# Kernel optimization log

Hardware: AMD Instinct MI355X
Metric: run time of the kernel (lower is better)

Reference implementation:

```python
import jax, jax.numpy as jnp
import numpy as np
import math

EMBED_DIM = 1024
NUM_HEADS = 16
HEAD_DIM = EMBED_DIM // NUM_HEADS
BLOCK_SIZE = 64
NUM_RAND_BLOCKS = 3
B, L = 2, 2048


def _build_sparse_mask(seq_len, block_size, num_rand_blocks, seed=0):
    """BigBird block-sparse mask: global (first/last block) + window (prev/self/next) + random blocks."""
    nb = seq_len // block_size
    bm = np.zeros((nb, nb), dtype=bool)
    # global: first and last blocks attend to all / are attended by all
    bm[0, :] = True
    bm[:, 0] = True
    bm[-1, :] = True
    bm[:, -1] = True
    # sliding window for interior blocks
    for b in range(1, nb - 1):
        bm[b, max(b - 1, 0):b + 2] = True
    # random blocks for interior blocks (deterministic for reproducibility)
    rng = np.random.default_rng(seed)
    for b in range(1, nb - 1):
        avail = [x for x in range(nb) if x != b]
        picks = rng.permutation(len(avail))[:num_rand_blocks]
        for p in picks:
            bm[b, avail[p]] = True
    # expand block mask to token-level [L, L]
    return np.kron(bm, np.ones((block_size, block_size), dtype=bool))


def setup_inputs() -> dict:
    key = jax.random.key(0)
    k0, k1, k2, k3, k4 = jax.random.split(key, 5)
    hidden_states = jax.random.normal(k0, (B, L, EMBED_DIM), dtype=jnp.float32)
    s = 0.02
    # torch nn.Linear weights have shape [out_features, in_features]
    Wq = jax.random.normal(k1, (EMBED_DIM, EMBED_DIM), dtype=jnp.float32) * s
    Wk = jax.random.normal(k2, (EMBED_DIM, EMBED_DIM), dtype=jnp.float32) * s
    Wv = jax.random.normal(k3, (EMBED_DIM, EMBED_DIM), dtype=jnp.float32) * s
    Wo = jax.random.normal(k4, (EMBED_DIM, EMBED_DIM), dtype=jnp.float32) * s
    sparse_mask = jnp.asarray(_build_sparse_mask(L, BLOCK_SIZE, NUM_RAND_BLOCKS))
    return {"hidden_states": hidden_states, "Wq": Wq, "Wk": Wk, "Wv": Wv,
            "Wo": Wo, "sparse_mask": sparse_mask}


def reference(hidden_states, Wq, Wk, Wv, Wo, sparse_mask):
    Bsz, Lq, D = hidden_states.shape
    H, hd = NUM_HEADS, HEAD_DIM
    # projections (Linear no bias): x @ W.T
    q = (hidden_states @ Wq.T).reshape(Bsz, Lq, H, hd).transpose(0, 2, 1, 3)
    k = (hidden_states @ Wk.T).reshape(Bsz, Lq, H, hd).transpose(0, 2, 1, 3)
    v = (hidden_states @ Wv.T).reshape(Bsz, Lq, H, hd).transpose(0, 2, 1, 3)
    # dense scores with block-sparse mask (matches reference module's math)
    scores = jnp.einsum('bhqd,bhkd->bhqk', q, k) / math.sqrt(hd)  # [B,H,L,L]
    scores = jnp.where(sparse_mask[None, None, :, :], scores, -jnp.inf)
    attn = jax.nn.softmax(scores.astype(jnp.float32), axis=-1).astype(scores.dtype)
    out = jnp.einsum('bhqk,bhkd->bhqd', attn, v)
    out = out.transpose(0, 2, 1, 3).reshape(Bsz, Lq, D)
    out = out @ Wo.T
    return out
```

## Files before the change

kernel.cpp:

```cpp
#include <hip/hip_runtime.h>
#include <hip/hip_bf16.h>
#include <stdint.h>

#define LSEQ   2048
#define DMODEL 1024
#define NHEADS 16
#define HDIM   64
#define NB     32
#define BATCH  2
#define NGRP   38
#define NWG_ATTN (32 * NGRP)

typedef unsigned short u16;
typedef __attribute__((ext_vector_type(8))) __bf16 bf16x8;
typedef __attribute__((ext_vector_type(4))) float f32x4;
typedef __attribute__((ext_vector_type(4))) unsigned int u32x4;
typedef __attribute__((ext_vector_type(4))) u16 u16x4;


__device__ __forceinline__ u16 f2b(float f) {
  unsigned b = __float_as_uint(f);
  return (u16)((b + 0x7FFFu + ((b >> 16) & 1u)) >> 16);
}

__device__ __forceinline__ void lds_dma16(const u16* g, u16* l) {
  __builtin_amdgcn_global_load_lds(
      (__attribute__((address_space(1))) const void*)g,
      (__attribute__((address_space(3))) void*)l, 16, 0, 0);
}

__device__ __forceinline__ bool probe_is_bf16(const void* src) {
  const u16* p = (const u16*)src;
  int cnt = 0;
  #pragma unroll
  for (int i = 0; i < 64; ++i) {
    int e = (p[i] >> 7) & 0xFF;
    cnt += (e >= 100 && e <= 140) ? 1 : 0;
  }
  return cnt >= 48;
}

__device__ __forceinline__ bool mask_block(const void* m, int qb, int kb) {
  const unsigned char* p = (const unsigned char*)m;
  size_t e = (size_t)(qb * 64) * LSEQ + (size_t)kb * 64;
  unsigned char b0 = p[0], b1 = p[1], b2 = p[2];
  if (b0 == 1 && b1 == 1) return p[e] != 0;
  if (b0 == 1 && b1 == 0 && b2 == 1) return ((const u16*)m)[e] != 0;
  if (b0 == 1) return ((const unsigned int*)m)[e] != 0;
  if (b0 == 0x80 && b1 == 0x3f) return ((const u16*)m)[e] != 0;
  return ((const float*)m)[e] != 0.0f;
}

__global__ __launch_bounds__(256) void convert_kernel(
    const void* __restrict__ hs, const void* __restrict__ wq,
    const void* __restrict__ wk, const void* __restrict__ wv,
    const void* __restrict__ wo, u16* __restrict__ dst,
    const void* __restrict__ mask, int* __restrict__ skb,
    f32x4* __restrict__ zbuf, int zn4) {
  if (blockIdx.x == 0 && threadIdx.x < NB) {
    int qb = threadIdx.x;
    int base = (qb == 0) ? 0 : ((qb == 31) ? 32 : (64 + (qb - 1) * 8));
    int cap = (qb == 0 || qb == 31) ? 32 : 8;
    int c = 0;
    for (int kb = 0; kb < NB; ++kb)
      if (mask_block(mask, qb, kb)) skb[base + c++] = kb;
    for (; c < cap; ++c) skb[base + c] = -1;
  }
  int stride = gridDim.x * blockDim.x;
  for (int i = blockIdx.x * blockDim.x + threadIdx.x; i < zn4; i += stride)
    zbuf[i] = (f32x4){0.f, 0.f, 0.f, 0.f};

  if (probe_is_bf16(hs)) return;

  const int HS4 = BATCH * LSEQ * DMODEL / 4;
  const int W4 = DMODEL * DMODEL / 4;
  int total4 = HS4 + 4 * W4;
  for (int i = blockIdx.x * blockDim.x + threadIdx.x; i < total4; i += stride) {
    const void* src;
    int off;
    if (i < HS4) { src = hs; off = i; }
    else {
      int j = i - HS4;
      int wsel = j >> 18;
      off = j & (W4 - 1);
      src = (wsel == 0) ? wq : (wsel == 1) ? wk : (wsel == 2) ? wv : wo;
    }
    f32x4 f = ((const f32x4*)src)[off];
    ((u16x4*)dst)[i] = (u16x4){f2b(f[0]), f2b(f[1]), f2b(f[2]), f2b(f[3])};
  }
}

#define GBK 32
#define TN  128

template <int TM>
__global__ __launch_bounds__(256) void gemm_bt(
    const void* __restrict__ probe_src,
    const u16* __restrict__ A_bf, const u16* __restrict__ A_alt,
    const u16* __restrict__ Braw0, const u16* __restrict__ Braw1,
    const u16* __restrict__ Braw2, const u16* __restrict__ Bconv,
    void* __restrict__ C, u16* __restrict__ C2, int N, int K, int layout) {
  constexpr int NJ = (TM == 128) ? 4 : 2;
  __shared__ u16 lA[TM * 32];
  __shared__ u16 lB[TN * 32];
  int t = threadIdx.x;
  int w = t >> 6, l = t & 63, q4 = l >> 4, lc = l & 15;
  int lr = l >> 2, lcc = l & 3;
  int tileM = blockIdx.x * TM, tileN = blockIdx.y * TN;
  int wm = (TM == 128) ? (w >> 1) * 64 : 0;
  int wn = (TM == 128) ? (w & 1) * 64 : w * 32;

  bool bf = probe_is_bf16(probe_src);
  const u16* A = bf ? A_bf : A_alt;
  const u16* Bbase;
  int bOff;
  if (bf) {
    Bbase = (tileN < 1024) ? Braw0 : (tileN < 2048) ? Braw1 : Braw2;
    bOff = tileN & 1023;
  } else {
    Bbase = Bconv;
    bOff = tileN;
  }

  f32x4 acc[4][NJ] = {};

  for (int kt = 0; kt < K; kt += GBK) {
    __syncthreads();
    #pragma unroll
    for (int it = 0; it < TM / 64; ++it) {
      int m = w * (TM / 64) + it;
      lds_dma16(A + (size_t)(tileM + m * 16 + lr) * K + kt + lcc * 8, lA + m * 512);
    }
    #pragma unroll
    for (int it = 0; it < 2; ++it) {
      int m = w * 2 + it;
      lds_dma16(Bbase + (size_t)(bOff + m * 16 + lr) * K + kt + lcc * 8, lB + m * 512);
    }
    __syncthreads();

    bf16x8 af[4], bfr[NJ];
    #pragma unroll
    for (int i = 0; i < 4; ++i)
      af[i] = *(const bf16x8*)(lA + (wm + i * 16 + lc) * 32 + q4 * 8);
    #pragma unroll
    for (int j = 0; j < NJ; ++j)
      bfr[j] = *(const bf16x8*)(lB + (wn + j * 16 + lc) * 32 + q4 * 8);
    #pragma unroll
    for (int i = 0; i < 4; ++i)
      #pragma unroll
      for (int j = 0; j < NJ; ++j)
        acc[i][j] = __builtin_amdgcn_mfma_f32_16x16x32_bf16(af[i], bfr[j], acc[i][j], 0, 0, 0);
  }

  bool out_bf = (layout == 1) ? true : bf;
  #pragma unroll
  for (int i = 0; i < 4; ++i)
    #pragma unroll
    for (int j = 0; j < NJ; ++j) {
      int rowb = tileM + wm + i * 16 + q4 * 4;
      int col = tileN + wn + j * 16 + lc;
      if (layout == 0) {
        #pragma unroll
        for (int r = 0; r < 4; ++r) {
          float v = acc[i][j][r];
          size_t idx = (size_t)(rowb + r) * N + col;
          if (out_bf) ((u16*)C)[idx] = f2b(v);
          else ((float*)C)[idx] = v;
        }
      } else {
        int sel = col >> 10;
        int o = col & 1023;
        int h = o >> 6, d = o & 63;
        int b = rowb >> 11, ll = rowb & 2047;
        if (sel == 2) {
          u16x4 pk = {f2b(acc[i][j][0]), f2b(acc[i][j][1]),
                      f2b(acc[i][j][2]), f2b(acc[i][j][3])};
          *(u16x4*)(C2 + ((size_t)((b * NHEADS + h) * HDIM + d)) * LSEQ + ll) = pk;
        } else {
          float sc = (sel == 0) ? 0.125f : 1.0f;
          #pragma unroll
          for (int r = 0; r < 4; ++r) {
            size_t idx = (size_t)sel * (size_t)(BATCH * NHEADS * LSEQ * HDIM) +
                         (((size_t)(b * NHEADS + h) * LSEQ) + ll + r) * HDIM + d;
            ((u16*)C)[idx] = f2b(acc[i][j][r] * sc);
          }
        }
      }
    }
}

#define LDP 72

__global__ __launch_bounds__(256) void attn_kernel(
    const u16* __restrict__ qb_, const u16* __restrict__ kb_,
    const u16* __restrict__ vt_, const int* __restrict__ skb,
    float* __restrict__ obuf2, float* __restrict__ lbuf2,
    u16* __restrict__ ctx) {
  __shared__ u16 lK[2][64 * 64];
  __shared__ u16 lV[2][64 * 64];
  __shared__ u16 lP[4][16 * LDP];
  int i = blockIdx.x;
  int bh = (i & 7) + ((i >> 3) & 3) * 8;
  int g = i >> 5;
  int qb = (g < 4) ? 0 : ((g < 8) ? 31 : (g - 7));
  int t = threadIdx.x, w = t >> 6, l = t & 63, q4 = l >> 4, lc = l & 15;
  int c0 = t, c1 = 256 + t;
  int r0 = c0 >> 3, cc0 = c0 & 7, r1 = c1 >> 3, cc1 = c1 & 7;

  const u16* qp = qb_ + ((size_t)bh * LSEQ + qb * 64 + w * 16 + lc) * HDIM;
  bf16x8 bq0 = *(const bf16x8*)(qp + q4 * 8);
  bf16x8 bq1 = *(const bf16x8*)(qp + 32 + q4 * 8);

  const u16* kp = kb_ + (size_t)bh * LSEQ * HDIM;
  const u16* vp = vt_ + (size_t)bh * HDIM * LSEQ;
  u16* myP = &lP[w][0];

  f32x4 oacc[4];
  #pragma unroll
  for (int d = 0; d < 4; ++d) oacc[d] = (f32x4){0.f, 0.f, 0.f, 0.f};
  float lp = 0.0f;

  for (int ph = 0; ph < 4; ++ph) {
    int kb0 = skb[g * 8 + 2 * ph];
    if (kb0 < 0) break;
    int kb1 = skb[g * 8 + 2 * ph + 1];
    int kb1e = (kb1 < 0) ? kb0 : kb1;

    __syncthreads();
    #pragma unroll
    for (int u = 0; u < 2; ++u) {
      int kbu = u ? kb1e : kb0;
      const u16* kblk = kp + (size_t)kbu * 64 * HDIM;
      const u16* vblk = vp + kbu * 64;
      lds_dma16(kblk + r0 * HDIM + cc0 * 8, lK[u] + w * 512);
      lds_dma16(kblk + r1 * HDIM + cc1 * 8, lK[u] + 2048 + w * 512);
      lds_dma16(vblk + (size_t)r0 * LSEQ + cc0 * 8, lV[u] + w * 512);
      lds_dma16(vblk + (size_t)r1 * LSEQ + cc1 * 8, lV[u] + 2048 + w * 512);
    }
    __syncthreads();

    #pragma unroll
    for (int u = 0; u < 2; ++u) {
      if (u == 1 && kb1 < 0) break;
      f32x4 st[4];
      #pragma unroll
      for (int mt = 0; mt < 4; ++mt) {
        bf16x8 k0 = *(const bf16x8*)(lK[u] + (mt * 16 + lc) * 64 + q4 * 8);
        bf16x8 k1 = *(const bf16x8*)(lK[u] + (mt * 16 + lc) * 64 + 32 + q4 * 8);
        f32x4 z = (f32x4){0.f, 0.f, 0.f, 0.f};
        z = __builtin_amdgcn_mfma_f32_16x16x32_bf16(k0, bq0, z, 0, 0, 0);
        z = __builtin_amdgcn_mfma_f32_16x16x32_bf16(k1, bq1, z, 0, 0, 0);
        st[mt] = z;
      }

      #pragma unroll
      for (int mt = 0; mt < 4; ++mt) {
        float p0 = __expf(st[mt][0]), p1 = __expf(st[mt][1]);
        float p2 = __expf(st[mt][2]), p3 = __expf(st[mt][3]);
        lp += (p0 + p1) + (p2 + p3);
        u16x4 pk = {f2b(p0), f2b(p1), f2b(p2), f2b(p3)};
        *(u16x4*)(myP + lc * LDP + mt * 16 + q4 * 4) = pk;
      }

      bf16x8 ap0 = *(const bf16x8*)(myP + lc * LDP + q4 * 8);
      bf16x8 ap1 = *(const bf16x8*)(myP + lc * LDP + 32 + q4 * 8);
      #pragma unroll
      for (int dt = 0; dt < 4; ++dt) {
        bf16x8 v0 = *(const bf16x8*)(lV[u] + (dt * 16 + lc) * 64 + q4 * 8);
        bf16x8 v1 = *(const bf16x8*)(lV[u] + (dt * 16 + lc) * 64 + 32 + q4 * 8);
        oacc[dt] = __builtin_amdgcn_mfma_f32_16x16x32_bf16(ap0, v0, oacc[dt], 0, 0, 0);
        oacc[dt] = __builtin_amdgcn_mfma_f32_16x16x32_bf16(ap1, v1, oacc[dt], 0, 0, 0);
      }
    }
  }

  float ltot = lp;
  ltot += __shfl_xor(ltot, 16);
  ltot += __shfl_xor(ltot, 32);

  if (g >= 8) {
    float inv[4];
    #pragma unroll
    for (int r = 0; r < 4; ++r)
      inv[r] = 1.0f / __shfl(ltot, q4 * 4 + r);
    int b = bh >> 4, h = bh & 15;
    #pragma unroll
    for (int dt = 0; dt < 4; ++dt)
      #pragma unroll
      for (int r = 0; r < 4; ++r) {
        float v = oacc[dt][r] * inv[r];
        int grow = qb * 64 + w * 16 + q4 * 4 + r;
        size_t odx = ((size_t)b * LSEQ + grow) * DMODEL + h * HDIM + dt * 16 + lc;
        ctx[odx] = f2b(v);
      }
  } else {
    int s = (qb == 31) ? 1 : 0;
    if (q4 == 0)
      unsafeAtomicAdd(lbuf2 + ((size_t)bh * 2 + s) * 64 + w * 16 + lc, ltot);
    #pragma unroll
    for (int dt = 0; dt < 4; ++dt)
      #pragma unroll
      for (int r = 0; r < 4; ++r)
        unsafeAtomicAdd(obuf2 + (((size_t)bh * 2 + s) * 64 + w * 16 + q4 * 4 + r) * 64 +
                            dt * 16 + lc, oacc[dt][r]);
  }
}

__global__ __launch_bounds__(256) void normalize2_kernel(
    const float* __restrict__ obuf2, const float* __restrict__ lbuf2,
    u16* __restrict__ ctx) {
  int e4 = blockIdx.x * 256 + threadIdx.x;
  int e = e4 * 4;
  int bh = e >> 13;
  int rem = e & 8191;
  int s = rem >> 12, row = (rem >> 6) & 63, d = rem & 63;
  f32x4 o = *(const f32x4*)(obuf2 + e);
  float linv = 1.0f / lbuf2[(bh * 2 + s) * 64 + row];
  int qb = s ? 31 : 0;
  int b = bh >> 4, h = bh & 15;
  int grow = qb * 64 + row;
  u16x4 pk = {f2b(o[0] * linv), f2b(o[1] * linv), f2b(o[2] * linv), f2b(o[3] * linv)};
  *(u16x4*)(ctx + ((size_t)b * LSEQ + grow) * DMODEL + h * HDIM + d) = pk;
}

extern "C" void kernel_launch(void* const* d_in, const int* in_sizes, int n_in,
                              void* d_out, int out_size, void* d_ws, size_t ws_size,
                              hipStream_t stream) {
  const void* hs = d_in[0];
  const u16* wq = (const u16*)d_in[1];
  const u16* wk = (const u16*)d_in[2];
  const u16* wv = (const u16*)d_in[3];
  const u16* wo = (const u16*)d_in[4];
  const void* mask = d_in[5];

  u16* hsb = (u16*)d_ws;
  u16* wqb = hsb + 4 * 1024 * 1024;
  u16* wob = wqb + 3 * 1024 * 1024;
  u16* qbuf = wob + 1024 * 1024;
  u16* kbuf = qbuf + 4 * 1024 * 1024;
  u16* vtb  = kbuf + 4 * 1024 * 1024;
  u16* ctx  = vtb + 4 * 1024 * 1024;
  int* skb  = (int*)(ctx + 4 * 1024 * 1024);
  float* obuf2 = (float*)(skb + 512);
  float* lbuf2 = obuf2 + 32 * 2 * 64 * 64;
  const int ZN4 = (32 * 2 * 64 * 64 + 4096) / 4;

  convert_kernel<<<4096, 256, 0, stream>>>(hs, wq, wk, wv, wo, hsb, mask, skb,
                                           (f32x4*)obuf2, ZN4);

  dim3 gqkv(32, 24);
  gemm_bt<128><<<gqkv, 256, 0, stream>>>(hs, (const u16*)hs, hsb,
                                         wq, wk, wv, wqb,
                                         qbuf, vtb, 3072, 1024, 1);

  attn_kernel<<<NWG_ATTN, 256, 0, stream>>>(qbuf, kbuf, vtb, skb, obuf2, lbuf2, ctx);

  normalize2_kernel<<<256, 256, 0, stream>>>(obuf2, lbuf2, ctx);

  dim3 gout(64, 8);
  gemm_bt<64><<<gout, 256, 0, stream>>>(hs, ctx, ctx,
                                        wo, wo, wo, wob,
                                        d_out, nullptr, 1024, 1024, 0);
}
```

Baseline: 213.5 us.

## Fuse normalization into attention and derive sparse block lists from mask in-kernel

Drops the separate normalize kernel. The last of the four global-row workgroups, found through an atomic counter, now divides the accumulated output by its denominator and writes the context directly. Instead of reading precomputed lists, each attention workgroup builds its list of active key blocks from the mask with a wave ballot, and zeroing of the accumulation buffers moves into the QKV GEMM. K/V staging is now single-buffered, one key block per sync pair instead of two. This trades a kernel launch and the serial list build for more barriers per workgroup and extra atomics and fences in the global-row workgroups.

```diff
diff --git a/kernel.cpp b/kernel.cpp
--- a/kernel.cpp
+++ b/kernel.cpp
@@ -51,30 +51,15 @@
   return ((const float*)m)[e] != 0.0f;
 }
 
-__global__ __launch_bounds__(256) void convert_kernel(
+__global__ __launch_bounds__(256) void prep_fp32(
     const void* __restrict__ hs, const void* __restrict__ wq,
     const void* __restrict__ wk, const void* __restrict__ wv,
-    const void* __restrict__ wo, u16* __restrict__ dst,
-    const void* __restrict__ mask, int* __restrict__ skb,
-    f32x4* __restrict__ zbuf, int zn4) {
-  if (blockIdx.x == 0 && threadIdx.x < NB) {
-    int qb = threadIdx.x;
-    int base = (qb == 0) ? 0 : ((qb == 31) ? 32 : (64 + (qb - 1) * 8));
-    int cap = (qb == 0 || qb == 31) ? 32 : 8;
-    int c = 0;
-    for (int kb = 0; kb < NB; ++kb)
-      if (mask_block(mask, qb, kb)) skb[base + c++] = kb;
-    for (; c < cap; ++c) skb[base + c] = -1;
-  }
-  int stride = gridDim.x * blockDim.x;
-  for (int i = blockIdx.x * blockDim.x + threadIdx.x; i < zn4; i += stride)
-    zbuf[i] = (f32x4){0.f, 0.f, 0.f, 0.f};
-
+    const void* __restrict__ wo, u16* __restrict__ dst) {
   if (probe_is_bf16(hs)) return;
-
   const int HS4 = BATCH * LSEQ * DMODEL / 4;
   const int W4 = DMODEL * DMODEL / 4;
   int total4 = HS4 + 4 * W4;
+  int stride = gridDim.x * blockDim.x;
   for (int i = blockIdx.x * blockDim.x + threadIdx.x; i < total4; i += stride) {
     const void* src;
     int off;
@@ -94,12 +79,10 @@
 #define TN  128
 
 template <int TM>
-__global__ __launch_bounds__(256) void gemm_bt(
-    const void* __restrict__ probe_src,
-    const u16* __restrict__ A_bf, const u16* __restrict__ A_alt,
-    const u16* __restrict__ Braw0, const u16* __restrict__ Braw1,
-    const u16* __restrict__ Braw2, const u16* __restrict__ Bconv,
-    void* __restrict__ C, u16* __restrict__ C2, int N, int K, int layout) {
+__device__ __forceinline__ void gemm_bt_body(
+    const u16* __restrict__ A, const u16* __restrict__ Bbase, int bOff,
+    void* __restrict__ C, u16* __restrict__ C2, int N, int K,
+    int layout, bool out_bf) {
   constexpr int NJ = (TM == 128) ? 4 : 2;
   __shared__ u16 lA[TM * 32];
   __shared__ u16 lB[TN * 32];
@@ -110,18 +93,6 @@
   int wm = (TM == 128) ? (w >> 1) * 64 : 0;
   int wn = (TM == 128) ? (w & 1) * 64 : w * 32;
 
-  bool bf = probe_is_bf16(probe_src);
-  const u16* A = bf ? A_bf : A_alt;
-  const u16* Bbase;
-  int bOff;
-  if (bf) {
-    Bbase = (tileN < 1024) ? Braw0 : (tileN < 2048) ? Braw1 : Braw2;
-    bOff = tileN & 1023;
-  } else {
-    Bbase = Bconv;
-    bOff = tileN;
-  }
-
   f32x4 acc[4][NJ] = {};
 
   for (int kt = 0; kt < K; kt += GBK) {
@@ -152,7 +123,6 @@
         acc[i][j] = __builtin_amdgcn_mfma_f32_16x16x32_bf16(af[i], bfr[j], acc[i][j], 0, 0, 0);
   }
 
-  bool out_bf = (layout == 1) ? true : bf;
   #pragma unroll
   for (int i = 0; i < 4; ++i)
     #pragma unroll
@@ -189,16 +159,49 @@
     }
 }
 
+__global__ __launch_bounds__(256) void gemm_qkv(
+    const void* __restrict__ hs, const u16* __restrict__ wq,
+    const u16* __restrict__ wk, const u16* __restrict__ wv,
+    const u16* __restrict__ hsb, const u16* __restrict__ wqb,
+    u16* __restrict__ qbuf, u16* __restrict__ vtb,
+    f32x4* __restrict__ zbuf, int zn4) {
+  int zi = (blockIdx.y * gridDim.x + blockIdx.x) * 256 + threadIdx.x;
+  if (zi < zn4) zbuf[zi] = (f32x4){0.f, 0.f, 0.f, 0.f};
+  bool bf = probe_is_bf16(hs);
+  const u16* A = bf ? (const u16*)hs : hsb;
+  int tileN = blockIdx.y * TN;
+  const u16* Bbase;
+  int bOff;
+  if (bf) {
+    Bbase = (tileN < 1024) ? wq : (tileN < 2048) ? wk : wv;
+    bOff = tileN & 1023;
+  } else {
+    Bbase = wqb;
+    bOff = tileN;
+  }
+  gemm_bt_body<128>(A, Bbase, bOff, qbuf, vtb, 3072, 1024, 1, true);
+}
+
+__global__ __launch_bounds__(256) void gemm_out(
+    const void* __restrict__ hs, const u16* __restrict__ ctx,
+    const u16* __restrict__ wo, const u16* __restrict__ wob,
+    void* __restrict__ dout) {
+  bool bf = probe_is_bf16(hs);
+  int tileN = blockIdx.y * TN;
+  gemm_bt_body<64>(ctx, bf ? wo : wob, tileN, dout, nullptr, 1024, 1024, 0, bf);
+}
+
 #define LDP 72
 
-__global__ __launch_bounds__(256) void attn_kernel(
+__global__ __launch_bounds__(256) void attn_sparse(
     const u16* __restrict__ qb_, const u16* __restrict__ kb_,
-    const u16* __restrict__ vt_, const int* __restrict__ skb,
+    const u16* __restrict__ vt_, const void* __restrict__ mask,
     float* __restrict__ obuf2, float* __restrict__ lbuf2,
-    u16* __restrict__ ctx) {
-  __shared__ u16 lK[2][64 * 64];
-  __shared__ u16 lV[2][64 * 64];
+    int* __restrict__ cnt, u16* __restrict__ ctx) {
+  __shared__ u16 lK[64 * 64];
+  __shared__ u16 lV[64 * 64];
   __shared__ u16 lP[4][16 * LDP];
+  __shared__ int slast;
   int i = blockIdx.x;
   int bh = (i & 7) + ((i >> 3) & 3) * 8;
   int g = i >> 5;
@@ -207,6 +210,11 @@
   int c0 = t, c1 = 256 + t;
   int r0 = c0 >> 3, cc0 = c0 & 7, r1 = c1 >> 3, cc1 = c1 & 7;
 
+  bool act = (l < NB) ? mask_block(mask, qb, l) : false;
+  unsigned bits = (unsigned)(__ballot(act) & 0xFFFFFFFFull);
+  int skip = (g < 8) ? (g & 3) * 8 : 0;
+  for (int s2 = 0; s2 < skip; ++s2) bits &= bits - 1;
+
   const u16* qp = qb_ + ((size_t)bh * LSEQ + qb * 64 + w * 16 + lc) * HDIM;
   bf16x8 bq0 = *(const bf16x8*)(qp + q4 * 8);
   bf16x8 bq1 = *(const bf16x8*)(qp + 32 + q4 * 8);
@@ -220,57 +228,46 @@
   for (int d = 0; d < 4; ++d) oacc[d] = (f32x4){0.f, 0.f, 0.f, 0.f};
   float lp = 0.0f;
 
-  for (int ph = 0; ph < 4; ++ph) {
-    int kb0 = skb[g * 8 + 2 * ph];
-    if (kb0 < 0) break;
-    int kb1 = skb[g * 8 + 2 * ph + 1];
-    int kb1e = (kb1 < 0) ? kb0 : kb1;
-
-    __syncthreads();
-    #pragma unroll
-    for (int u = 0; u < 2; ++u) {
-      int kbu = u ? kb1e : kb0;
-      const u16* kblk = kp + (size_t)kbu * 64 * HDIM;
-      const u16* vblk = vp + kbu * 64;
-      lds_dma16(kblk + r0 * HDIM + cc0 * 8, lK[u] + w * 512);
-      lds_dma16(kblk + r1 * HDIM + cc1 * 8, lK[u] + 2048 + w * 512);
-      lds_dma16(vblk + (size_t)r0 * LSEQ + cc0 * 8, lV[u] + w * 512);
-      lds_dma16(vblk + (size_t)r1 * LSEQ + cc1 * 8, lV[u] + 2048 + w * 512);
-    }
-    __syncthreads();
-
-    #pragma unroll
-    for (int u = 0; u < 2; ++u) {
-      if (u == 1 && kb1 < 0) break;
-      f32x4 st[4];
-      #pragma unroll
-      for (int mt = 0; mt < 4; ++mt) {
-        bf16x8 k0 = *(const bf16x8*)(lK[u] + (mt * 16 + lc) * 64 + q4 * 8);
-        bf16x8 k1 = *(const bf16x8*)(lK[u] + (mt * 16 + lc) * 64 + 32 + q4 * 8);
-        f32x4 z = (f32x4){0.f, 0.f, 0.f, 0.f};
-        z = __builtin_amdgcn_mfma_f32_16x16x32_bf16(k0, bq0, z, 0, 0, 0);
-        z = __builtin_amdgcn_mfma_f32_16x16x32_bf16(k1, bq1, z, 0, 0, 0);
-        st[mt] = z;
-      }
-
-      #pragma unroll
-      for (int mt = 0; mt < 4; ++mt) {
-        float p0 = __expf(st[mt][0]), p1 = __expf(st[mt][1]);
-        float p2 = __expf(st[mt][2]), p3 = __expf(st[mt][3]);
-        lp += (p0 + p1) + (p2 + p3);
-        u16x4 pk = {f2b(p0), f2b(p1), f2b(p2), f2b(p3)};
-        *(u16x4*)(myP + lc * LDP + mt * 16 + q4 * 4) = pk;
-      }
-
-      bf16x8 ap0 = *(const bf16x8*)(myP + lc * LDP + q4 * 8);
-      bf16x8 ap1 = *(const bf16x8*)(myP + lc * LDP + 32 + q4 * 8);
-      #pragma unroll
-      for (int dt = 0; dt < 4; ++dt) {
-        bf16x8 v0 = *(const bf16x8*)(lV[u] + (dt * 16 + lc) * 64 + q4 * 8);
-        bf16x8 v1 = *(const bf16x8*)(lV[u] + (dt * 16 + lc) * 64 + 32 + q4 * 8);
-        oacc[dt] = __builtin_amdgcn_mfma_f32_16x16x32_bf16(ap0, v0, oacc[dt], 0, 0, 0);
-        oacc[dt] = __builtin_amdgcn_mfma_f32_16x16x32_bf16(ap1, v1, oacc[dt], 0, 0, 0);
-      }
+  for (int it = 0; it < 8 && bits; ++it) {
+    int kb = __builtin_ctz(bits);
+    bits &= bits - 1;
+    const u16* kblk = kp + (size_t)kb * 64 * HDIM;
+    const u16* vblk = vp + kb * 64;
+    __syncthreads();
+    lds_dma16(kblk + r0 * HDIM + cc0 * 8, lK + w * 512);
+    lds_dma16(kblk + r1 * HDIM + cc1 * 8, lK + 2048 + w * 512);
+    lds_dma16(vblk + (size_t)r0 * LSEQ + cc0 * 8, lV + w * 512);
+    lds_dma16(vblk + (size_t)r1 * LSEQ + cc1 * 8, lV + 2048 + w * 512);
+    __syncthreads();
+
+    f32x4 st[4];
+    #pragma unroll
+    for (int mt = 0; mt < 4; ++mt) {
+      bf16x8 k0 = *(const bf16x8*)(lK + (mt * 16 + lc) * 64 + q4 * 8);
+      bf16x8 k1 = *(const bf16x8*)(lK + (mt * 16 + lc) * 64 + 32 + q4 * 8);
+      f32x4 z = (f32x4){0.f, 0.f, 0.f, 0.f};
+      z = __builtin_amdgcn_mfma_f32_16x16x32_bf16(k0, bq0, z, 0, 0, 0);
+      z = __builtin_amdgcn_mfma_f32_16x16x32_bf16(k1, bq1, z, 0, 0, 0);
+      st[mt] = z;
+    }
+
+    #pragma unroll
+    for (int mt = 0; mt < 4; ++mt) {
+      float p0 = __expf(st[mt][0]), p1 = __expf(st[mt][1]);
+      float p2 = __expf(st[mt][2]), p3 = __expf(st[mt][3]);
+      lp += (p0 + p1) + (p2 + p3);
+      u16x4 pk = {f2b(p0), f2b(p1), f2b(p2), f2b(p3)};
+      *(u16x4*)(myP + lc * LDP + mt * 16 + q4 * 4) = pk;
+    }
+
+    bf16x8 ap0 = *(const bf16x8*)(myP + lc * LDP + q4 * 8);
+    bf16x8 ap1 = *(const bf16x8*)(myP + lc * LDP + 32 + q4 * 8);
+    #pragma unroll
+    for (int dt = 0; dt < 4; ++dt) {
+      bf16x8 v0 = *(const bf16x8*)(lV + (dt * 16 + lc) * 64 + q4 * 8);
+      bf16x8 v1 = *(const bf16x8*)(lV + (dt * 16 + lc) * 64 + 32 + q4 * 8);
+      oacc[dt] = __builtin_amdgcn_mfma_f32_16x16x32_bf16(ap0, v0, oacc[dt], 0, 0, 0);
+      oacc[dt] = __builtin_amdgcn_mfma_f32_16x16x32_bf16(ap1, v1, oacc[dt], 0, 0, 0);
     }
   }
 
@@ -295,32 +292,31 @@
       }
   } else {
     int s = (qb == 31) ? 1 : 0;
-    if (q4 == 0)
-      unsafeAtomicAdd(lbuf2 + ((size_t)bh * 2 + s) * 64 + w * 16 + lc, ltot);
+    int bs = bh * 2 + s;
+    float* ob = obuf2 + (size_t)bs * 4096;
+    float* lb = lbuf2 + bs * 64;
+    if (q4 == 0) unsafeAtomicAdd(lb + w * 16 + lc, ltot);
     #pragma unroll
     for (int dt = 0; dt < 4; ++dt)
       #pragma unroll
       for (int r = 0; r < 4; ++r)
-        unsafeAtomicAdd(obuf2 + (((size_t)bh * 2 + s) * 64 + w * 16 + q4 * 4 + r) * 64 +
-                            dt * 16 + lc, oacc[dt][r]);
-  }
-}
-
-__global__ __launch_bounds__(256) void normalize2_kernel(
-    const float* __restrict__ obuf2, const float* __restrict__ lbuf2,
-    u16* __restrict__ ctx) {
-  int e4 = blockIdx.x * 256 + threadIdx.x;
-  int e = e4 * 4;
-  int bh = e >> 13;
-  int rem = e & 8191;
-  int s = rem >> 12, row = (rem >> 6) & 63, d = rem & 63;
-  f32x4 o = *(const f32x4*)(obuf2 + e);
-  float linv = 1.0f / lbuf2[(bh * 2 + s) * 64 + row];
-  int qb = s ? 31 : 0;
-  int b = bh >> 4, h = bh & 15;
-  int grow = qb * 64 + row;
-  u16x4 pk = {f2b(o[0] * linv), f2b(o[1] * linv), f2b(o[2] * linv), f2b(o[3] * linv)};
-  *(u16x4*)(ctx + ((size_t)b * LSEQ + grow) * DMODEL + h * HDIM + d) = pk;
+        unsafeAtomicAdd(ob + (w * 16 + q4 * 4 + r) * 64 + dt * 16 + lc, oacc[dt][r]);
+
+    __threadfence();
+    if (t == 0) slast = (atomicAdd(cnt + bs, 1) == 3) ? 1 : 0;
+    __syncthreads();
+    if (slast) {
+      int b = bh >> 4, h = bh & 15;
+      for (int e = t; e < 4096; e += 256) {
+        int row = e >> 6, d = e & 63;
+        float o = unsafeAtomicAdd(ob + e, 0.0f);
+        float lden = unsafeAtomicAdd(lb + row, 0.0f);
+        int grow = qb * 64 + row;
+        size_t odx = ((size_t)b * LSEQ + grow) * DMODEL + h * HDIM + d;
+        ctx[odx] = f2b(o / lden);
+      }
+    }
+  }
 }
 
 extern "C" void kernel_launch(void* const* d_in, const int* in_sizes, int n_in,
@@ -340,25 +336,20 @@
   u16* kbuf = qbuf + 4 * 1024 * 1024;
   u16* vtb  = kbuf + 4 * 1024 * 1024;
   u16* ctx  = vtb + 4 * 1024 * 1024;
-  int* skb  = (int*)(ctx + 4 * 1024 * 1024);
-  float* obuf2 = (float*)(skb + 512);
+  float* obuf2 = (float*)(ctx + 4 * 1024 * 1024);
   float* lbuf2 = obuf2 + 32 * 2 * 64 * 64;
-  const int ZN4 = (32 * 2 * 64 * 64 + 4096) / 4;
-
-  convert_kernel<<<4096, 256, 0, stream>>>(hs, wq, wk, wv, wo, hsb, mask, skb,
-                                           (f32x4*)obuf2, ZN4);
+  int* cnt = (int*)(lbuf2 + 4096);
+  const int ZN4 = (32 * 2 * 64 * 64 + 4096 + 64) / 4;
+
+  prep_fp32<<<2048, 256, 0, stream>>>(hs, wq, wk, wv, wo, hsb);
 
   dim3 gqkv(32, 24);
-  gemm_bt<128><<<gqkv, 256, 0, stream>>>(hs, (const u16*)hs, hsb,
-                                         wq, wk, wv, wqb,
-                                         qbuf, vtb, 3072, 1024, 1);
-
-  attn_kernel<<<NWG_ATTN, 256, 0, stream>>>(qbuf, kbuf, vtb, skb, obuf2, lbuf2, ctx);
-
-  normalize2_kernel<<<256, 256, 0, stream>>>(obuf2, lbuf2, ctx);
+  gemm_qkv<<<gqkv, 256, 0, stream>>>(hs, wq, wk, wv, hsb, wqb, qbuf, vtb,
+                                     (f32x4*)obuf2, ZN4);
+
+  attn_sparse<<<NWG_ATTN, 256, 0, stream>>>(qbuf, kbuf, vtb, mask,
+                                            obuf2, lbuf2, cnt, ctx);
 
   dim3 gout(64, 8);
-  gemm_bt<64><<<gout, 256, 0, stream>>>(hs, ctx, ctx,
-                                        wo, wo, wo, wob,
-                                        d_out, nullptr, 1024, 1024, 0);
-}
+  gemm_out<<<gout, 256, 0, stream>>>(hs, ctx, wo, wob, d_out);
+}
```

Result: slower. 320.7 us (+50.2%).
